# Performance work log

Hardware: AMD Instinct MI355X
Metric: run time of the kernel (lower is better)

The kernel has to match this reference:

```python
import jax, jax.numpy as jnp
import numpy as np

B, S, D, H = 4, 2048, 512, 8
HD = D // H  # head dim = 64


def setup_inputs() -> dict:
    key = jax.random.key(0)
    ks = jax.random.split(key, 7)
    s = 0.02
    return {
        "X": jax.random.normal(ks[0], (B, S, D), dtype=jnp.float32),
        "Y": jax.random.normal(ks[1], (B, S, D), dtype=jnp.float32),
        "Z": jax.random.normal(ks[2], (B, S, D), dtype=jnp.float32),
        # weights stored as [in, out] (torch Linear weight transposed)
        "Wq": jax.random.normal(ks[3], (D, D), dtype=jnp.float32) * s,
        "Wk": jax.random.normal(ks[4], (D, D), dtype=jnp.float32) * s,
        "Wv": jax.random.normal(ks[5], (D, D), dtype=jnp.float32) * s,  # dead in original forward
        "Wo": jax.random.normal(ks[6], (D, D), dtype=jnp.float32) * s,
    }


def _split_heads(t):
    # [B, S, D] -> [B, H, S, HD]
    return t.reshape(B, S, H, HD).transpose(0, 2, 1, 3)


def reference(X, Y, Z, Wq, Wk, Wv, Wo):
    q = _split_heads(X @ Wq)
    k = _split_heads(Y @ Wk)
    # NOTE: original module (faithfully) uses W_o for the value projection; W_v is unused.
    v = _split_heads(Z @ Wo)
    scores = jnp.einsum("bhqd,bhkd->bhqk", q, k) / jnp.sqrt(jnp.float32(HD))
    # sigmoid(s) > 0.5  <=>  s > 0 (sigmoid strictly monotone); keep score else 0
    scores = jnp.where(scores > 0, scores, jnp.float32(0))
    attn = jax.nn.softmax(scores, axis=-1)
    out = jnp.einsum("bhqk,bhkd->bhqd", attn, v)  # dropout inactive at eval
    out = out.transpose(0, 2, 1, 3).reshape(B, S, D)  # merge heads
    return out @ Wo
```

## Files before the change

kernel.cpp:

```cpp
#include <hip/hip_runtime.h>
#include <math.h>

#define S_LEN 2048
#define DIM   512
#define M_TOT 8192
#define NCH   (S_LEN / 64)

typedef __attribute__((ext_vector_type(8))) short bf16x8;
typedef __attribute__((ext_vector_type(4))) short bf16x4;
typedef __attribute__((ext_vector_type(4))) float f32x4;

#define MFMA(a, b, c) __builtin_amdgcn_mfma_f32_16x16x32_bf16((a), (b), (c), 0, 0, 0)

__device__ __forceinline__ short f2b(float x) {
    union { float f; unsigned u; } v; v.f = x;
    unsigned r = v.u + 0x7FFFu + ((v.u >> 16) & 1u);
    return (short)(r >> 16);
}

__global__ __launch_bounds__(256) void cvt_bf16(const float* __restrict__ X,
                                                const float* __restrict__ Y,
                                                const float* __restrict__ Z,
                                                short* __restrict__ Xb,
                                                short* __restrict__ Yb,
                                                short* __restrict__ Zb) {
    const int zi = blockIdx.y;
    const float* A = zi == 0 ? X : zi == 1 ? Y : Z;
    short* O = zi == 0 ? Xb : zi == 1 ? Yb : Zb;
    const size_t i = (size_t)blockIdx.x * 256 + threadIdx.x;
    float4 a = ((const float4*)A)[2 * i];
    float4 b = ((const float4*)A)[2 * i + 1];
    bf16x8 o = { f2b(a.x), f2b(a.y), f2b(a.z), f2b(a.w),
                 f2b(b.x), f2b(b.y), f2b(b.z), f2b(b.w) };
    *(bf16x8*)&O[i * 8] = o;
}

__global__ __launch_bounds__(256) void prep_wt(const float* Wq, const float* Wk, const float* Wo,
                                               short* Wtq, short* Wtk, short* Wto) {
    const int zi = blockIdx.z;
    const float* W = zi == 0 ? Wq : zi == 1 ? Wk : Wo;
    short*      Wt = zi == 0 ? Wtq : zi == 1 ? Wtk : Wto;
    __shared__ short Ts[64 * 72];
    const int t = threadIdx.x;
    const int k0 = blockIdx.x * 64, n0 = blockIdx.y * 64;
    #pragma unroll
    for (int it = 0; it < 4; ++it) {
        const int r = (t >> 4) + 16 * it;
        const int cq = t & 15;
        float4 v = *(const float4*)&W[(size_t)(k0 + r) * DIM + n0 + cq * 4];
        Ts[(4 * cq + 0) * 72 + r] = f2b(v.x);
        Ts[(4 * cq + 1) * 72 + r] = f2b(v.y);
        Ts[(4 * cq + 2) * 72 + r] = f2b(v.z);
        Ts[(4 * cq + 3) * 72 + r] = f2b(v.w);
    }
    __syncthreads();
    #pragma unroll
    for (int it = 0; it < 2; ++it) {
        const int n = (t >> 3) + 32 * it;
        const int sg = t & 7;
        *(bf16x8*)&Wt[(size_t)(n0 + n) * DIM + k0 + sg * 8] = *(const bf16x8*)&Ts[n * 72 + sg * 8];
    }
}

__global__ __launch_bounds__(256) void proj_gemm(const short* __restrict__ Xb,
                                                 const short* __restrict__ Yb,
                                                 const short* __restrict__ Zb,
                                                 const short* __restrict__ Wtq,
                                                 const short* __restrict__ Wtk,
                                                 const short* __restrict__ Wto,
                                                 short* __restrict__ Qb,
                                                 short* __restrict__ Kb,
                                                 short* __restrict__ Vt) {
    const int zi = blockIdx.z;
    const short* A  = zi == 0 ? Xb : zi == 1 ? Yb : Zb;
    const short* Bw = zi == 0 ? Wtq : zi == 1 ? Wtk : Wto;

    __shared__ short As[128 * 40];
    __shared__ short Bs[128 * 40];
    const int tid = threadIdx.x;
    const int w = tid >> 6, ln = tid & 63, l15 = ln & 15, quad = ln >> 4;
    const int m0 = blockIdx.x * 128, n0 = blockIdx.y * 128;
    const int wm = (w & 1) * 64, wn = (w >> 1) * 64;

    const int r0 = tid >> 2, r1 = r0 + 64;
    const int sg = tid & 3;
    const short* ap0 = A  + (size_t)(m0 + r0) * DIM + sg * 8;
    const short* ap1 = A  + (size_t)(m0 + r1) * DIM + sg * 8;
    const short* bp0 = Bw + (size_t)(n0 + r0) * DIM + sg * 8;
    const short* bp1 = Bw + (size_t)(n0 + r1) * DIM + sg * 8;

    bf16x8 a0 = *(const bf16x8*)ap0, a1 = *(const bf16x8*)ap1;
    bf16x8 b0 = *(const bf16x8*)bp0, b1 = *(const bf16x8*)bp1;

    f32x4 acc[4][4] = {};

    for (int k0 = 0; k0 < DIM; k0 += 32) {
        __syncthreads();
        *(bf16x8*)&As[r0 * 40 + sg * 8] = a0;
        *(bf16x8*)&As[r1 * 40 + sg * 8] = a1;
        *(bf16x8*)&Bs[r0 * 40 + sg * 8] = b0;
        *(bf16x8*)&Bs[r1 * 40 + sg * 8] = b1;
        __syncthreads();
        const int kn = (k0 + 32 < DIM) ? k0 + 32 : 0;
        a0 = *(const bf16x8*)(ap0 + kn); a1 = *(const bf16x8*)(ap1 + kn);
        b0 = *(const bf16x8*)(bp0 + kn); b1 = *(const bf16x8*)(bp1 + kn);

        bf16x8 af[4], bf[4];
        #pragma unroll
        for (int mf = 0; mf < 4; ++mf) af[mf] = *(const bf16x8*)&As[(wm + 16 * mf + l15) * 40 + quad * 8];
        #pragma unroll
        for (int nf = 0; nf < 4; ++nf) bf[nf] = *(const bf16x8*)&Bs[(wn + 16 * nf + l15) * 40 + quad * 8];
        #pragma unroll
        for (int mf = 0; mf < 4; ++mf)
            #pragma unroll
            for (int nf = 0; nf < 4; ++nf)
                acc[mf][nf] = MFMA(af[mf], bf[nf], acc[mf][nf]);
    }

    if (zi < 2) {
        short* C = zi == 0 ? Qb : Kb;
        #pragma unroll
        for (int mf = 0; mf < 4; ++mf)
            #pragma unroll
            for (int nf = 0; nf < 4; ++nf)
                #pragma unroll
                for (int r = 0; r < 4; ++r)
                    C[(size_t)(m0 + wm + 16 * mf + 4 * quad + r) * DIM + n0 + wn + 16 * nf + l15] =
                        f2b(acc[mf][nf][r]);
    } else {
        #pragma unroll
        for (int mf = 0; mf < 4; ++mf)
            #pragma unroll
            for (int nf = 0; nf < 4; ++nf) {
                const int col = n0 + wn + 16 * nf + l15;
                const int h = col >> 6, hd = col & 63;
                const int row0_ = m0 + wm + 16 * mf + 4 * quad;
                const int bb = row0_ >> 11, s0 = row0_ & 2047;
                bf16x4 o = { f2b(acc[mf][nf][0]), f2b(acc[mf][nf][1]),
                             f2b(acc[mf][nf][2]), f2b(acc[mf][nf][3]) };
                *(bf16x4*)&Vt[((size_t)((bb * 8 + h) * 64 + hd)) * S_LEN + s0] = o;
            }
    }
}

__global__ __launch_bounds__(256) void out_gemm(const short* __restrict__ Ob,
                                                const short* __restrict__ Wto,
                                                float* __restrict__ Cout) {
    __shared__ short As[128 * 40];
    __shared__ short Bs[128 * 40];
    const int tid = threadIdx.x;
    const int w = tid >> 6, ln = tid & 63, l15 = ln & 15, quad = ln >> 4;
    const int m0 = blockIdx.x * 128, n0 = blockIdx.y * 128;
    const int wm = (w & 1) * 64, wn = (w >> 1) * 64;

    const int r0 = tid >> 2, r1 = r0 + 64;
    const int sg = tid & 3;
    const short* ap0 = Ob  + (size_t)(m0 + r0) * DIM + sg * 8;
    const short* ap1 = Ob  + (size_t)(m0 + r1) * DIM + sg * 8;
    const short* bp0 = Wto + (size_t)(n0 + r0) * DIM + sg * 8;
    const short* bp1 = Wto + (size_t)(n0 + r1) * DIM + sg * 8;

    bf16x8 a0 = *(const bf16x8*)ap0, a1 = *(const bf16x8*)ap1;
    bf16x8 b0 = *(const bf16x8*)bp0, b1 = *(const bf16x8*)bp1;

    f32x4 acc[4][4] = {};

    for (int k0 = 0; k0 < DIM; k0 += 32) {
        __syncthreads();
        *(bf16x8*)&As[r0 * 40 + sg * 8] = a0;
        *(bf16x8*)&As[r1 * 40 + sg * 8] = a1;
        *(bf16x8*)&Bs[r0 * 40 + sg * 8] = b0;
        *(bf16x8*)&Bs[r1 * 40 + sg * 8] = b1;
        __syncthreads();
        const int kn = (k0 + 32 < DIM) ? k0 + 32 : 0;
        a0 = *(const bf16x8*)(ap0 + kn); a1 = *(const bf16x8*)(ap1 + kn);
        b0 = *(const bf16x8*)(bp0 + kn); b1 = *(const bf16x8*)(bp1 + kn);

        bf16x8 af[4], bf[4];
        #pragma unroll
        for (int mf = 0; mf < 4; ++mf) af[mf] = *(const bf16x8*)&As[(wm + 16 * mf + l15) * 40 + quad * 8];
        #pragma unroll
        for (int nf = 0; nf < 4; ++nf) bf[nf] = *(const bf16x8*)&Bs[(wn + 16 * nf + l15) * 40 + quad * 8];
        #pragma unroll
        for (int mf = 0; mf < 4; ++mf)
            #pragma unroll
            for (int nf = 0; nf < 4; ++nf)
                acc[mf][nf] = MFMA(af[mf], bf[nf], acc[mf][nf]);
    }
    #pragma unroll
    for (int mf = 0; mf < 4; ++mf)
        #pragma unroll
        for (int nf = 0; nf < 4; ++nf)
            #pragma unroll
            for (int r = 0; r < 4; ++r)
                Cout[(size_t)(m0 + wm + 16 * mf + 4 * quad + r) * DIM + n0 + wn + 16 * nf + l15] =
                    acc[mf][nf][r];
}

__global__ __launch_bounds__(256) void attn_mfma(const short* __restrict__ Qb,
                                                 const short* __restrict__ Kb,
                                                 const short* __restrict__ Vtg,
                                                 short* __restrict__ Ob) {
    __shared__ short Ks[2][64 * 72];
    __shared__ short Vs[2][64 * 72];
    __shared__ short Es[4][32 * 72];

    const int tid = threadIdx.x;
    const int w = tid >> 6, ln = tid & 63, l15 = ln & 15, quad = ln >> 4;
    const int qt0 = blockIdx.x * 128;
    const int bh = blockIdx.y, b = bh >> 3, h = bh & 7;
    const size_t tokbase = (size_t)b * S_LEN;

    bf16x8 qf[2][2];
    #pragma unroll
    for (int nf = 0; nf < 2; ++nf)
        #pragma unroll
        for (int ks = 0; ks < 2; ++ks)
            qf[nf][ks] = *(const bf16x8*)&Qb[(tokbase + qt0 + 32 * w + 16 * nf + l15) * DIM +
                                             h * 64 + 32 * ks + 8 * quad];

    const int srow = tid >> 3, ssg = tid & 7;
    const short* kbase = Kb  + (tokbase + srow) * DIM + h * 64 + ssg * 8;
    const short* vbase = Vtg + ((size_t)bh * 64 + srow) * S_LEN + ssg * 8;

    bf16x8 k0r, k1r, v0r, v1r;

    f32x4 oacc[2][4] = {};
    float dsum[2] = {0.f, 0.f};

    {
        k0r = *(const bf16x8*)kbase;
        k1r = *(const bf16x8*)(kbase + (size_t)32 * DIM);
        v0r = *(const bf16x8*)vbase;
        v1r = *(const bf16x8*)(vbase + (size_t)32 * S_LEN);
        *(bf16x8*)&Ks[0][srow * 72 + ssg * 8] = k0r;
        *(bf16x8*)&Ks[0][(srow + 32) * 72 + ssg * 8] = k1r;
        *(bf16x8*)&Vs[0][srow * 72 + ssg * 8] = v0r;
        *(bf16x8*)&Vs[0][(srow + 32) * 72 + ssg * 8] = v1r;
        k0r = *(const bf16x8*)(kbase + (size_t)64 * DIM);
        k1r = *(const bf16x8*)(kbase + (size_t)96 * DIM);
        v0r = *(const bf16x8*)(vbase + 64);
        v1r = *(const bf16x8*)(vbase + (size_t)32 * S_LEN + 64);
    }
    __syncthreads();

    for (int kc = 0; kc < NCH; ++kc) {
        const int cur = kc & 1;
        if (kc + 1 < NCH) {
            *(bf16x8*)&Ks[cur ^ 1][srow * 72 + ssg * 8] = k0r;
            *(bf16x8*)&Ks[cur ^ 1][(srow + 32) * 72 + ssg * 8] = k1r;
            *(bf16x8*)&Vs[cur ^ 1][srow * 72 + ssg * 8] = v0r;
            *(bf16x8*)&Vs[cur ^ 1][(srow + 32) * 72 + ssg * 8] = v1r;
        }
        if (kc + 2 < NCH) {
            const size_t ko = (size_t)(kc + 2) * 64 * DIM;
            const size_t vo = (size_t)(kc + 2) * 64;
            k0r = *(const bf16x8*)(kbase + ko);
            k1r = *(const bf16x8*)(kbase + ko + (size_t)32 * DIM);
            v0r = *(const bf16x8*)(vbase + vo);
            v1r = *(const bf16x8*)(vbase + vo + (size_t)32 * S_LEN);
        }

        f32x4 sacc[4][2];
        #pragma unroll
        for (int mf = 0; mf < 4; ++mf) {
            bf16x8 ka = *(const bf16x8*)&Ks[cur][(16 * mf + l15) * 72 + 8 * quad];
            bf16x8 kb = *(const bf16x8*)&Ks[cur][(16 * mf + l15) * 72 + 32 + 8 * quad];
            #pragma unroll
            for (int nf = 0; nf < 2; ++nf) {
                f32x4 s = {0.f, 0.f, 0.f, 0.f};
                s = MFMA(ka, qf[nf][0], s);
                s = MFMA(kb, qf[nf][1], s);
                sacc[mf][nf] = s;
            }
        }

        short* Esw = &Es[w][0];
        #pragma unroll
        for (int mf = 0; mf < 4; ++mf)
            #pragma unroll
            for (int nf = 0; nf < 2; ++nf) {
                bf16x4 e4;
                #pragma unroll
                for (int r = 0; r < 4; ++r) {
                    const float e = __expf(fmaxf(sacc[mf][nf][r], 0.f) * 0.125f);
                    dsum[nf] += e;
                    e4[r] = f2b(e);
                }
                *(bf16x4*)&Esw[(16 * nf + l15) * 72 + 16 * mf + 4 * quad] = e4;
            }

        bf16x8 e00 = *(const bf16x8*)&Esw[l15 * 72 + 8 * quad];
        bf16x8 e01 = *(const bf16x8*)&Esw[l15 * 72 + 32 + 8 * quad];
        bf16x8 e10 = *(const bf16x8*)&Esw[(16 + l15) * 72 + 8 * quad];
        bf16x8 e11 = *(const bf16x8*)&Esw[(16 + l15) * 72 + 32 + 8 * quad];
        #pragma unroll
        for (int nf2 = 0; nf2 < 4; ++nf2) {
            bf16x8 vf0 = *(const bf16x8*)&Vs[cur][(16 * nf2 + l15) * 72 + 8 * quad];
            bf16x8 vf1 = *(const bf16x8*)&Vs[cur][(16 * nf2 + l15) * 72 + 32 + 8 * quad];
            oacc[0][nf2] = MFMA(e00, vf0, oacc[0][nf2]);
            oacc[0][nf2] = MFMA(e01, vf1, oacc[0][nf2]);
            oacc[1][nf2] = MFMA(e10, vf0, oacc[1][nf2]);
            oacc[1][nf2] = MFMA(e11, vf1, oacc[1][nf2]);
        }
        __syncthreads();
    }

    #pragma unroll
    for (int nf = 0; nf < 2; ++nf) {
        dsum[nf] += __shfl_xor(dsum[nf], 16);
        dsum[nf] += __shfl_xor(dsum[nf], 32);
    }
    const float dinv0 = 1.0f / dsum[0];
    const float dinv1 = 1.0f / dsum[1];

    #pragma unroll
    for (int mf2 = 0; mf2 < 2; ++mf2) {
        const float dv = mf2 ? dinv1 : dinv0;
        #pragma unroll
        for (int r = 0; r < 4; ++r) {
            const float di = __shfl(dv, 4 * quad + r);
            const size_t rowaddr = (tokbase + qt0 + 32 * w + 16 * mf2 + 4 * quad + r) * DIM + h * 64;
            #pragma unroll
            for (int nf2 = 0; nf2 < 4; ++nf2)
                Ob[rowaddr + 16 * nf2 + l15] = f2b(oacc[mf2][nf2][r] * di);
        }
    }
}

extern "C" void kernel_launch(void* const* d_in, const int* in_sizes, int n_in,
                              void* d_out, int out_size, void* d_ws, size_t ws_size,
                              hipStream_t stream) {
    const float* X  = (const float*)d_in[0];
    const float* Y  = (const float*)d_in[1];
    const float* Z  = (const float*)d_in[2];
    const float* Wq = (const float*)d_in[3];
    const float* Wk = (const float*)d_in[4];
    const float* Wo = (const float*)d_in[6];

    char* p = (char*)d_ws;
    const size_t MD = (size_t)M_TOT * DIM;
    short* Qb  = (short*)p; p += MD * 2;
    short* Kb  = (short*)p; p += MD * 2;
    short* Vt  = (short*)p; p += MD * 2;
    short* Ob  = (short*)p; p += MD * 2;
    short* Xb  = (short*)p; p += MD * 2;
    short* Yb  = (short*)p; p += MD * 2;
    short* Zb  = (short*)p; p += MD * 2;
    short* Wtq = (short*)p; p += (size_t)DIM * DIM * 2;
    short* Wtk = (short*)p; p += (size_t)DIM * DIM * 2;
    short* Wto = (short*)p; p += (size_t)DIM * DIM * 2;

    cvt_bf16<<<dim3(M_TOT * DIM / 8 / 256, 3), 256, 0, stream>>>(X, Y, Z, Xb, Yb, Zb);
    prep_wt<<<dim3(8, 8, 3), 256, 0, stream>>>(Wq, Wk, Wo, Wtq, Wtk, Wto);
    proj_gemm<<<dim3(64, 4, 3), 256, 0, stream>>>(Xb, Yb, Zb, Wtq, Wtk, Wto, Qb, Kb, Vt);
    attn_mfma<<<dim3(16, 32), 256, 0, stream>>>(Qb, Kb, Vt, Ob);
    out_gemm<<<dim3(64, 4), 256, 0, stream>>>(Ob, Wto, (float*)d_out);
}
```

Baseline: 215.8 us.

## Fuse input bf16 conversion into projection GEMM and restructure attention to 8 waves

Drops the standalone fp32-to-bf16 conversion kernel: the projection GEMM now loads fp32 X/Y/Z directly and packs them to bf16 when staging to shared memory. Folds the softmax scale and log2(e) into Q so attention can use exp2. The attention kernel is rebuilt as 512 threads with 16 query rows per wave, and the row sum is computed with an MFMA against a ones vector. Rounding is simplified to round-half-up, and LDS padding shrinks to 68, which makes the 16-byte LDS reads only 8-byte aligned. Expected costs are extra global bytes in the GEMM A loads and possible bank or alignment penalties.

```diff
diff --git a/kernel.cpp b/kernel.cpp
--- a/kernel.cpp
+++ b/kernel.cpp
@@ -12,27 +12,15 @@
 
 #define MFMA(a, b, c) __builtin_amdgcn_mfma_f32_16x16x32_bf16((a), (b), (c), 0, 0, 0)
 
+#define QSCALE 0.18033688f
+
 __device__ __forceinline__ short f2b(float x) {
     union { float f; unsigned u; } v; v.f = x;
-    unsigned r = v.u + 0x7FFFu + ((v.u >> 16) & 1u);
-    return (short)(r >> 16);
-}
-
-__global__ __launch_bounds__(256) void cvt_bf16(const float* __restrict__ X,
-                                                const float* __restrict__ Y,
-                                                const float* __restrict__ Z,
-                                                short* __restrict__ Xb,
-                                                short* __restrict__ Yb,
-                                                short* __restrict__ Zb) {
-    const int zi = blockIdx.y;
-    const float* A = zi == 0 ? X : zi == 1 ? Y : Z;
-    short* O = zi == 0 ? Xb : zi == 1 ? Yb : Zb;
-    const size_t i = (size_t)blockIdx.x * 256 + threadIdx.x;
-    float4 a = ((const float4*)A)[2 * i];
-    float4 b = ((const float4*)A)[2 * i + 1];
-    bf16x8 o = { f2b(a.x), f2b(a.y), f2b(a.z), f2b(a.w),
-                 f2b(b.x), f2b(b.y), f2b(b.z), f2b(b.w) };
-    *(bf16x8*)&O[i * 8] = o;
+    return (short)((v.u + 0x8000u) >> 16);
+}
+__device__ __forceinline__ int pack2(float x, float y) {
+    union { float f; unsigned u; } a, b; a.f = x; b.f = y;
+    return __builtin_amdgcn_perm(b.u + 0x8000u, a.u + 0x8000u, 0x07060302u);
 }
 
 __global__ __launch_bounds__(256) void prep_wt(const float* Wq, const float* Wk, const float* Wo,
@@ -62,9 +50,9 @@
     }
 }
 
-__global__ __launch_bounds__(256) void proj_gemm(const short* __restrict__ Xb,
-                                                 const short* __restrict__ Yb,
-                                                 const short* __restrict__ Zb,
+__global__ __launch_bounds__(256) void proj_gemm(const float* __restrict__ X,
+                                                 const float* __restrict__ Y,
+                                                 const float* __restrict__ Z,
                                                  const short* __restrict__ Wtq,
                                                  const short* __restrict__ Wtk,
                                                  const short* __restrict__ Wto,
@@ -72,7 +60,7 @@
                                                  short* __restrict__ Kb,
                                                  short* __restrict__ Vt) {
     const int zi = blockIdx.z;
-    const short* A  = zi == 0 ? Xb : zi == 1 ? Yb : Zb;
+    const float* A  = zi == 0 ? X : zi == 1 ? Y : Z;
     const short* Bw = zi == 0 ? Wtq : zi == 1 ? Wtk : Wto;
 
     __shared__ short As[128 * 40];
@@ -84,25 +72,33 @@
 
     const int r0 = tid >> 2, r1 = r0 + 64;
     const int sg = tid & 3;
-    const short* ap0 = A  + (size_t)(m0 + r0) * DIM + sg * 8;
-    const short* ap1 = A  + (size_t)(m0 + r1) * DIM + sg * 8;
+    const float* ap0 = A  + (size_t)(m0 + r0) * DIM + sg * 8;
+    const float* ap1 = A  + (size_t)(m0 + r1) * DIM + sg * 8;
     const short* bp0 = Bw + (size_t)(n0 + r0) * DIM + sg * 8;
     const short* bp1 = Bw + (size_t)(n0 + r1) * DIM + sg * 8;
 
-    bf16x8 a0 = *(const bf16x8*)ap0, a1 = *(const bf16x8*)ap1;
+    float4 a0a = *(const float4*)ap0, a0b = *(const float4*)(ap0 + 4);
+    float4 a1a = *(const float4*)ap1, a1b = *(const float4*)(ap1 + 4);
     bf16x8 b0 = *(const bf16x8*)bp0, b1 = *(const bf16x8*)bp1;
 
     f32x4 acc[4][4] = {};
 
     for (int k0 = 0; k0 < DIM; k0 += 32) {
         __syncthreads();
-        *(bf16x8*)&As[r0 * 40 + sg * 8] = a0;
-        *(bf16x8*)&As[r1 * 40 + sg * 8] = a1;
-        *(bf16x8*)&Bs[r0 * 40 + sg * 8] = b0;
-        *(bf16x8*)&Bs[r1 * 40 + sg * 8] = b1;
+        {
+            int4 p0 = { pack2(a0a.x, a0a.y), pack2(a0a.z, a0a.w),
+                        pack2(a0b.x, a0b.y), pack2(a0b.z, a0b.w) };
+            int4 p1 = { pack2(a1a.x, a1a.y), pack2(a1a.z, a1a.w),
+                        pack2(a1b.x, a1b.y), pack2(a1b.z, a1b.w) };
+            *(int4*)&As[r0 * 40 + sg * 8] = p0;
+            *(int4*)&As[r1 * 40 + sg * 8] = p1;
+            *(bf16x8*)&Bs[r0 * 40 + sg * 8] = b0;
+            *(bf16x8*)&Bs[r1 * 40 + sg * 8] = b1;
+        }
         __syncthreads();
         const int kn = (k0 + 32 < DIM) ? k0 + 32 : 0;
-        a0 = *(const bf16x8*)(ap0 + kn); a1 = *(const bf16x8*)(ap1 + kn);
+        a0a = *(const float4*)(ap0 + kn); a0b = *(const float4*)(ap0 + kn + 4);
+        a1a = *(const float4*)(ap1 + kn); a1b = *(const float4*)(ap1 + kn + 4);
         b0 = *(const bf16x8*)(bp0 + kn); b1 = *(const bf16x8*)(bp1 + kn);
 
         bf16x8 af[4], bf[4];
@@ -119,6 +115,7 @@
 
     if (zi < 2) {
         short* C = zi == 0 ? Qb : Kb;
+        const float scale = zi == 0 ? QSCALE : 1.0f;
         #pragma unroll
         for (int mf = 0; mf < 4; ++mf)
             #pragma unroll
@@ -126,7 +123,7 @@
                 #pragma unroll
                 for (int r = 0; r < 4; ++r)
                     C[(size_t)(m0 + wm + 16 * mf + 4 * quad + r) * DIM + n0 + wn + 16 * nf + l15] =
-                        f2b(acc[mf][nf][r]);
+                        f2b(acc[mf][nf][r] * scale);
     } else {
         #pragma unroll
         for (int mf = 0; mf < 4; ++mf)
@@ -136,9 +133,9 @@
                 const int h = col >> 6, hd = col & 63;
                 const int row0_ = m0 + wm + 16 * mf + 4 * quad;
                 const int bb = row0_ >> 11, s0 = row0_ & 2047;
-                bf16x4 o = { f2b(acc[mf][nf][0]), f2b(acc[mf][nf][1]),
-                             f2b(acc[mf][nf][2]), f2b(acc[mf][nf][3]) };
-                *(bf16x4*)&Vt[((size_t)((bb * 8 + h) * 64 + hd)) * S_LEN + s0] = o;
+                int2 o = { pack2(acc[mf][nf][0], acc[mf][nf][1]),
+                           pack2(acc[mf][nf][2], acc[mf][nf][3]) };
+                *(int2*)&Vt[((size_t)((bb * 8 + h) * 64 + hd)) * S_LEN + s0] = o;
             }
     }
 }
@@ -197,13 +194,13 @@
                     acc[mf][nf][r];
 }
 
-__global__ __launch_bounds__(256) void attn_mfma(const short* __restrict__ Qb,
+__global__ __launch_bounds__(512) void attn_mfma(const short* __restrict__ Qb,
                                                  const short* __restrict__ Kb,
                                                  const short* __restrict__ Vtg,
                                                  short* __restrict__ Ob) {
-    __shared__ short Ks[2][64 * 72];
-    __shared__ short Vs[2][64 * 72];
-    __shared__ short Es[4][32 * 72];
+    __shared__ short Ks[2][64 * 68];
+    __shared__ short Vs[2][64 * 68];
+    __shared__ short Es[8][16 * 68];
 
     const int tid = threadIdx.x;
     const int w = tid >> 6, ln = tid & 63, l15 = ln & 15, quad = ln >> 4;
@@ -211,120 +208,82 @@
     const int bh = blockIdx.y, b = bh >> 3, h = bh & 7;
     const size_t tokbase = (size_t)b * S_LEN;
 
-    bf16x8 qf[2][2];
-    #pragma unroll
-    for (int nf = 0; nf < 2; ++nf)
-        #pragma unroll
-        for (int ks = 0; ks < 2; ++ks)
-            qf[nf][ks] = *(const bf16x8*)&Qb[(tokbase + qt0 + 32 * w + 16 * nf + l15) * DIM +
-                                             h * 64 + 32 * ks + 8 * quad];
+    const size_t qrow = (tokbase + qt0 + 16 * w + l15) * DIM + h * 64 + 8 * quad;
+    bf16x8 qf0 = *(const bf16x8*)&Qb[qrow];
+    bf16x8 qf1 = *(const bf16x8*)&Qb[qrow + 32];
 
     const int srow = tid >> 3, ssg = tid & 7;
     const short* kbase = Kb  + (tokbase + srow) * DIM + h * 64 + ssg * 8;
     const short* vbase = Vtg + ((size_t)bh * 64 + srow) * S_LEN + ssg * 8;
 
-    bf16x8 k0r, k1r, v0r, v1r;
-
-    f32x4 oacc[2][4] = {};
-    float dsum[2] = {0.f, 0.f};
-
-    {
-        k0r = *(const bf16x8*)kbase;
-        k1r = *(const bf16x8*)(kbase + (size_t)32 * DIM);
-        v0r = *(const bf16x8*)vbase;
-        v1r = *(const bf16x8*)(vbase + (size_t)32 * S_LEN);
-        *(bf16x8*)&Ks[0][srow * 72 + ssg * 8] = k0r;
-        *(bf16x8*)&Ks[0][(srow + 32) * 72 + ssg * 8] = k1r;
-        *(bf16x8*)&Vs[0][srow * 72 + ssg * 8] = v0r;
-        *(bf16x8*)&Vs[0][(srow + 32) * 72 + ssg * 8] = v1r;
-        k0r = *(const bf16x8*)(kbase + (size_t)64 * DIM);
-        k1r = *(const bf16x8*)(kbase + (size_t)96 * DIM);
-        v0r = *(const bf16x8*)(vbase + 64);
-        v1r = *(const bf16x8*)(vbase + (size_t)32 * S_LEN + 64);
-    }
+    const bf16x8 ones = { 0x3F80, 0x3F80, 0x3F80, 0x3F80, 0x3F80, 0x3F80, 0x3F80, 0x3F80 };
+
+    f32x4 oacc[4] = {};
+    f32x4 dacc = {0.f, 0.f, 0.f, 0.f};
+
+    bf16x8 kr, vr;
+    kr = *(const bf16x8*)kbase;
+    vr = *(const bf16x8*)vbase;
+    *(bf16x8*)&Ks[0][srow * 68 + ssg * 8] = kr;
+    *(bf16x8*)&Vs[0][srow * 68 + ssg * 8] = vr;
+    kr = *(const bf16x8*)(kbase + (size_t)64 * DIM);
+    vr = *(const bf16x8*)(vbase + 64);
     __syncthreads();
 
     for (int kc = 0; kc < NCH; ++kc) {
         const int cur = kc & 1;
         if (kc + 1 < NCH) {
-            *(bf16x8*)&Ks[cur ^ 1][srow * 72 + ssg * 8] = k0r;
-            *(bf16x8*)&Ks[cur ^ 1][(srow + 32) * 72 + ssg * 8] = k1r;
-            *(bf16x8*)&Vs[cur ^ 1][srow * 72 + ssg * 8] = v0r;
-            *(bf16x8*)&Vs[cur ^ 1][(srow + 32) * 72 + ssg * 8] = v1r;
+            *(bf16x8*)&Ks[cur ^ 1][srow * 68 + ssg * 8] = kr;
+            *(bf16x8*)&Vs[cur ^ 1][srow * 68 + ssg * 8] = vr;
         }
         if (kc + 2 < NCH) {
-            const size_t ko = (size_t)(kc + 2) * 64 * DIM;
-            const size_t vo = (size_t)(kc + 2) * 64;
-            k0r = *(const bf16x8*)(kbase + ko);
-            k1r = *(const bf16x8*)(kbase + ko + (size_t)32 * DIM);
-            v0r = *(const bf16x8*)(vbase + vo);
-            v1r = *(const bf16x8*)(vbase + vo + (size_t)32 * S_LEN);
-        }
-
-        f32x4 sacc[4][2];
+            kr = *(const bf16x8*)(kbase + (size_t)(kc + 2) * 64 * DIM);
+            vr = *(const bf16x8*)(vbase + (size_t)(kc + 2) * 64);
+        }
+
+        f32x4 sacc[4];
         #pragma unroll
         for (int mf = 0; mf < 4; ++mf) {
-            bf16x8 ka = *(const bf16x8*)&Ks[cur][(16 * mf + l15) * 72 + 8 * quad];
-            bf16x8 kb = *(const bf16x8*)&Ks[cur][(16 * mf + l15) * 72 + 32 + 8 * quad];
-            #pragma unroll
-            for (int nf = 0; nf < 2; ++nf) {
-                f32x4 s = {0.f, 0.f, 0.f, 0.f};
-                s = MFMA(ka, qf[nf][0], s);
-                s = MFMA(kb, qf[nf][1], s);
-                sacc[mf][nf] = s;
-            }
+            bf16x8 ka = *(const bf16x8*)&Ks[cur][(16 * mf + l15) * 68 + 8 * quad];
+            bf16x8 kb2 = *(const bf16x8*)&Ks[cur][(16 * mf + l15) * 68 + 32 + 8 * quad];
+            f32x4 s = {0.f, 0.f, 0.f, 0.f};
+            s = MFMA(ka, qf0, s);
+            s = MFMA(kb2, qf1, s);
+            sacc[mf] = s;
         }
 
         short* Esw = &Es[w][0];
         #pragma unroll
-        for (int mf = 0; mf < 4; ++mf)
-            #pragma unroll
-            for (int nf = 0; nf < 2; ++nf) {
-                bf16x4 e4;
-                #pragma unroll
-                for (int r = 0; r < 4; ++r) {
-                    const float e = __expf(fmaxf(sacc[mf][nf][r], 0.f) * 0.125f);
-                    dsum[nf] += e;
-                    e4[r] = f2b(e);
-                }
-                *(bf16x4*)&Esw[(16 * nf + l15) * 72 + 16 * mf + 4 * quad] = e4;
-            }
-
-        bf16x8 e00 = *(const bf16x8*)&Esw[l15 * 72 + 8 * quad];
-        bf16x8 e01 = *(const bf16x8*)&Esw[l15 * 72 + 32 + 8 * quad];
-        bf16x8 e10 = *(const bf16x8*)&Esw[(16 + l15) * 72 + 8 * quad];
-        bf16x8 e11 = *(const bf16x8*)&Esw[(16 + l15) * 72 + 32 + 8 * quad];
+        for (int mf = 0; mf < 4; ++mf) {
+            float e0 = __builtin_amdgcn_exp2f(fmaxf(sacc[mf][0], 0.f));
+            float e1 = __builtin_amdgcn_exp2f(fmaxf(sacc[mf][1], 0.f));
+            float e2 = __builtin_amdgcn_exp2f(fmaxf(sacc[mf][2], 0.f));
+            float e3 = __builtin_amdgcn_exp2f(fmaxf(sacc[mf][3], 0.f));
+            int2 p = { pack2(e0, e1), pack2(e2, e3) };
+            *(int2*)&Esw[l15 * 68 + 16 * mf + 4 * quad] = p;
+        }
+
+        bf16x8 e0 = *(const bf16x8*)&Esw[l15 * 68 + 8 * quad];
+        bf16x8 e1 = *(const bf16x8*)&Esw[l15 * 68 + 32 + 8 * quad];
+        dacc = MFMA(e0, ones, dacc);
+        dacc = MFMA(e1, ones, dacc);
         #pragma unroll
         for (int nf2 = 0; nf2 < 4; ++nf2) {
-            bf16x8 vf0 = *(const bf16x8*)&Vs[cur][(16 * nf2 + l15) * 72 + 8 * quad];
-            bf16x8 vf1 = *(const bf16x8*)&Vs[cur][(16 * nf2 + l15) * 72 + 32 + 8 * quad];
-            oacc[0][nf2] = MFMA(e00, vf0, oacc[0][nf2]);
-            oacc[0][nf2] = MFMA(e01, vf1, oacc[0][nf2]);
-            oacc[1][nf2] = MFMA(e10, vf0, oacc[1][nf2]);
-            oacc[1][nf2] = MFMA(e11, vf1, oacc[1][nf2]);
+            bf16x8 vf0 = *(const bf16x8*)&Vs[cur][(16 * nf2 + l15) * 68 + 8 * quad];
+            bf16x8 vf1 = *(const bf16x8*)&Vs[cur][(16 * nf2 + l15) * 68 + 32 + 8 * quad];
+            oacc[nf2] = MFMA(e0, vf0, oacc[nf2]);
+            oacc[nf2] = MFMA(e1, vf1, oacc[nf2]);
         }
         __syncthreads();
     }
 
     #pragma unroll
-    for (int nf = 0; nf < 2; ++nf) {
-        dsum[nf] += __shfl_xor(dsum[nf], 16);
-        dsum[nf] += __shfl_xor(dsum[nf], 32);
-    }
-    const float dinv0 = 1.0f / dsum[0];
-    const float dinv1 = 1.0f / dsum[1];
-
-    #pragma unroll
-    for (int mf2 = 0; mf2 < 2; ++mf2) {
-        const float dv = mf2 ? dinv1 : dinv0;
-        #pragma unroll
-        for (int r = 0; r < 4; ++r) {
-            const float di = __shfl(dv, 4 * quad + r);
-            const size_t rowaddr = (tokbase + qt0 + 32 * w + 16 * mf2 + 4 * quad + r) * DIM + h * 64;
-            #pragma unroll
-            for (int nf2 = 0; nf2 < 4; ++nf2)
-                Ob[rowaddr + 16 * nf2 + l15] = f2b(oacc[mf2][nf2][r] * di);
-        }
+    for (int r = 0; r < 4; ++r) {
+        const float di = __builtin_amdgcn_rcpf(dacc[r]);
+        const size_t rowaddr = (tokbase + qt0 + 16 * w + 4 * quad + r) * DIM + h * 64;
+        #pragma unroll
+        for (int nf2 = 0; nf2 < 4; ++nf2)
+            Ob[rowaddr + 16 * nf2 + l15] = f2b(oacc[nf2][r] * di);
     }
 }
 
@@ -344,16 +303,12 @@
     short* Kb  = (short*)p; p += MD * 2;
     short* Vt  = (short*)p; p += MD * 2;
     short* Ob  = (short*)p; p += MD * 2;
-    short* Xb  = (short*)p; p += MD * 2;
-    short* Yb  = (short*)p; p += MD * 2;
-    short* Zb  = (short*)p; p += MD * 2;
     short* Wtq = (short*)p; p += (size_t)DIM * DIM * 2;
     short* Wtk = (short*)p; p += (size_t)DIM * DIM * 2;
     short* Wto = (short*)p; p += (size_t)DIM * DIM * 2;
 
-    cvt_bf16<<<dim3(M_TOT * DIM / 8 / 256, 3), 256, 0, stream>>>(X, Y, Z, Xb, Yb, Zb);
     prep_wt<<<dim3(8, 8, 3), 256, 0, stream>>>(Wq, Wk, Wo, Wtq, Wtk, Wto);
-    proj_gemm<<<dim3(64, 4, 3), 256, 0, stream>>>(Xb, Yb, Zb, Wtq, Wtk, Wto, Qb, Kb, Vt);
-    attn_mfma<<<dim3(16, 32), 256, 0, stream>>>(Qb, Kb, Vt, Ob);
+    proj_gemm<<<dim3(64, 4, 3), 256, 0, stream>>>(X, Y, Z, Wtq, Wtk, Wto, Qb, Kb, Vt);
+    attn_mfma<<<dim3(16, 32), 512, 0, stream>>>(Qb, Kb, Vt, Ob);
     out_gemm<<<dim3(64, 4), 256, 0, stream>>>(Ob, Wto, (float*)d_out);
 }
```

Result: slower. 224.2 us (+3.9%).
